# Kernel optimization log

Hardware: AMD Instinct MI355X
Metric: run time of the kernel (lower is better)

Reference implementation:

```python
import jax, jax.numpy as jnp
import numpy as np

B, S, D, H, IT, V = 2, 1024, 1024, 8, 28, 50257
DH = D // H
EPS = jnp.float32(1.1920929e-07)  # torch RMSNorm default eps = finfo(float32).eps


def _rmsnorm(x, w):
    # torch nn.RMSNorm: x * rsqrt(mean(x^2) + eps) * weight
    ms = jnp.mean(jnp.square(x), axis=-1, keepdims=True)
    return x * jax.lax.rsqrt(ms + EPS) * w


def setup_inputs() -> dict:
    key = jax.random.key(0)
    ks = jax.random.split(key, 8)
    s = 0.02
    tokens = jax.random.randint(ks[0], (B, S), 0, V)
    embed = jax.random.normal(ks[1], (V, D), dtype=jnp.float32) * s
    Wk = jax.random.normal(ks[2], (D, D), dtype=jnp.float32) * s
    Wv = jax.random.normal(ks[3], (D, D), dtype=jnp.float32) * s
    Ws = jax.random.normal(ks[4], (D, D), dtype=jnp.float32) * s
    Wo = jax.random.normal(ks[5], (D, D), dtype=jnp.float32) * s  # original zero-inits; randomized for a non-trivial baseline
    step_size = jnp.linspace(0.5, 0.1, IT, dtype=jnp.float32)
    norm_w = jnp.ones((IT, D), jnp.float32)   # per-iteration RMSNorm weight
    gamma = jnp.ones((IT, D), jnp.float32)
    beta = jnp.zeros((IT, D), jnp.float32)
    out_norm_w = jnp.ones((D,), jnp.float32)
    lm_head_w = jax.random.normal(ks[6], (V, D), dtype=jnp.float32) * s
    return dict(tokens=tokens, embed=embed, Wk=Wk, Wv=Wv, Ws=Ws, Wo=Wo,
                step_size=step_size, norm_w=norm_w, gamma=gamma, beta=beta,
                out_norm_w=out_norm_w, lm_head_w=lm_head_w)


def _forward(tokens, embed, Wk, Wv, Ws, Wo, step_size, norm_w, gamma, beta, out_norm_w, lm_head_w):
    b, s = tokens.shape
    causal = jnp.tril(jnp.ones((s, s), dtype=bool))  # allow j <= i
    scale = 1.0 / np.sqrt(DH)

    def compute_force(h):
        k = (h @ Wk.T).reshape(b, s, H, DH)
        v = (h @ Wv.T).reshape(b, s, H, DH)
        energy = jnp.einsum('bihd,bjhd->bhij', k, k) * scale
        logits = jnp.where(causal, -energy, -jnp.inf)  # softmax(-energy) with causal masking
        w = jax.nn.softmax(logits, axis=-1)
        pairwise = jnp.einsum('bhij,bjhd->bihd', w, v).reshape(b, s, D)
        return (pairwise + h @ Ws.T) @ Wo.T

    def step(x, p):
        st, nw, g, bb = p
        h = _rmsnorm(x, nw) * g + bb
        return x + compute_force(h) * st, None

    x0 = embed[tokens].astype(jnp.float32)
    x, _ = jax.lax.scan(jax.checkpoint(step), x0, (step_size, norm_w, gamma, beta))
    x = _rmsnorm(x, out_norm_w)
    return x @ lm_head_w.T  # [B, S, V] logits


def reference(tokens, embed, Wk, Wv, Ws, Wo, step_size, norm_w, gamma, beta, out_norm_w, lm_head_w):
    return _forward(tokens, embed, Wk, Wv, Ws, Wo, step_size, norm_w, gamma, beta, out_norm_w, lm_head_w)
```

## Files before the change

### kernel.cpp

```cpp
#include <hip/hip_runtime.h>
#include <cstdint>
#include <cstddef>

#define S_   1024
#define D_   1024
#define H_   8
#define DH_  128
#define IT_  28
#define V_   50257
#define B_   2
#define ROWS 2048
#define EPS_ 1.1920929e-07f

typedef unsigned short u16;
typedef __attribute__((ext_vector_type(8))) short s8v;
typedef __attribute__((ext_vector_type(4))) float f4v;

#define VMCNT0 asm volatile("s_waitcnt vmcnt(0)" ::: "memory")
#define LGKM0  asm volatile("s_waitcnt lgkmcnt(0)" ::: "memory")
#define RBAR   do { __builtin_amdgcn_s_barrier(); asm volatile("" ::: "memory"); } while (0)

static __device__ __forceinline__ void gload16(const void* g, void* l) {
  __builtin_amdgcn_global_load_lds((__attribute__((address_space(1))) void*)(g),
                                   (__attribute__((address_space(3))) void*)(l), 16, 0, 0);
}

static __device__ __forceinline__ u16 f2bf(float f) {
  union { float f; uint32_t u; } v; v.f = f;
  return (u16)((v.u + 0x7FFFu + ((v.u >> 16) & 1u)) >> 16);
}

static __device__ __forceinline__ float wave_sum(float v) {
#pragma unroll
  for (int o = 32; o > 0; o >>= 1) v += __shfl_xor(v, o, 64);
  return v;
}

__device__ __constant__ int IT_TAB[40] = {
  15,15,15,15, 14,14,14, 13,13,13, 12,12,12, 11,11,11,
  10,10, 9,9, 8,8, 7,7, 6, 5, 4, 3,
  14,10,6,2, 13,9,5,1, 12,8,4,0};
__device__ __constant__ int CH_TAB[40] = {
  0,1,2,3, 0,1,2, 0,1,2, 0,1,2, 0,1,2,
  0,1, 0,1, 0,1, 0,1, 0, 0, 0, 0,
  3,2,1,0, 3,2,1,0, 3,2,1,0};

__global__ __launch_bounds__(256) void k_embed(const int* __restrict__ tok,
                                               const float* __restrict__ emb,
                                               float* __restrict__ x) {
  const int row = blockIdx.x;
  const int t = tok[row];
  ((float4*)(x + (size_t)row * D_))[threadIdx.x] =
      ((const float4*)(emb + (size_t)t * D_))[threadIdx.x];
}

__global__ __launch_bounds__(256) void k_cvt(const float* __restrict__ w,
                                             u16* __restrict__ o, int n4) {
  const int idx = blockIdx.x * 256 + threadIdx.x;
  if (idx < n4) {
    const float4 f = ((const float4*)w)[idx];
    ushort4 u;
    u.x = f2bf(f.x); u.y = f2bf(f.y); u.z = f2bf(f.z); u.w = f2bf(f.w);
    ((ushort4*)o)[idx] = u;
  }
}

__global__ __launch_bounds__(256) void k_rmsnorm(const float* __restrict__ x,
                                                 const float* __restrict__ nw,
                                                 const float* __restrict__ g,
                                                 const float* __restrict__ bb,
                                                 u16* __restrict__ h) {
  const int row = blockIdx.x;
  const int tid = threadIdx.x;
  const float4 xv = ((const float4*)(x + (size_t)row * D_))[tid];
  float ss = xv.x*xv.x + xv.y*xv.y + xv.z*xv.z + xv.w*xv.w;
  ss = wave_sum(ss);
  __shared__ float red[4];
  const int lane = tid & 63, wid = tid >> 6;
  if (lane == 0) red[wid] = ss;
  __syncthreads();
  const float tot = red[0] + red[1] + red[2] + red[3];
  const float r = rsqrtf(tot * (1.0f / (float)D_) + EPS_);
  const float4 wv = ((const float4*)nw)[tid];
  float o[4];
  o[0] = xv.x * r * wv.x; o[1] = xv.y * r * wv.y;
  o[2] = xv.z * r * wv.z; o[3] = xv.w * r * wv.w;
  if (g) {
    const float4 gv = ((const float4*)g)[tid];
    const float4 bv = ((const float4*)bb)[tid];
    o[0] = o[0]*gv.x + bv.x; o[1] = o[1]*gv.y + bv.y;
    o[2] = o[2]*gv.z + bv.z; o[3] = o[3]*gv.w + bv.w;
  }
  ushort4 u;
  u.x = f2bf(o[0]); u.y = f2bf(o[1]); u.z = f2bf(o[2]); u.w = f2bf(o[3]);
  ((ushort4*)(h + (size_t)row * D_))[tid] = u;
}

template<int EPI, int SWAP, int NB>
__global__ __launch_bounds__(256) void k_gemm(const u16* __restrict__ A, int lda,
                                              const u16* __restrict__ Bm, int ldb,
                                              float* __restrict__ C, int ldc,
                                              int N, int K,
                                              const float* __restrict__ alphap, int aidx) {
  __shared__ u16 As0[128 * 32], As1[128 * 32];
  __shared__ u16 Bs0[64 * NB * 32], Bs1[64 * NB * 32];
  const int i0 = (SWAP ? blockIdx.x : blockIdx.y) * 128;
  const int j0 = (SWAP ? blockIdx.y : blockIdx.x) * (64 * NB);
  const int tid = threadIdx.x;
  const int lane = tid & 63, w = tid >> 6;
  const int wr = w >> 1, wc = w & 1;
  const int l15 = lane & 15, l4 = lane >> 4;
  const int ar = tid >> 2, ak = (tid & 3) << 3;
  int bj0 = j0 + ar;      if (bj0 > N - 1) bj0 = N - 1;
  int bj1 = j0 + ar + 64; if (bj1 > N - 1) bj1 = N - 1;

  f4v acc[4][2 * NB];
#pragma unroll
  for (int m = 0; m < 4; ++m)
#pragma unroll
    for (int n = 0; n < 2 * NB; ++n) acc[m][n] = (f4v)0.0f;

  auto STAGE = [&](u16* AsB, u16* BsB, int k0) {
    gload16(A + (size_t)(i0 + ar) * lda + k0 + ak, AsB + (size_t)tid * 8);
    gload16(A + (size_t)(i0 + ar + 64) * lda + k0 + ak, AsB + ((size_t)tid + 256) * 8);
    gload16(Bm + (size_t)bj0 * ldb + k0 + ak, BsB + (size_t)tid * 8);
    if (NB == 2)
      gload16(Bm + (size_t)bj1 * ldb + k0 + ak, BsB + ((size_t)tid + 256) * 8);
  };
  auto COMP = [&](const u16* AsB, const u16* BsB) {
    s8v a[4], b[2 * NB];
#pragma unroll
    for (int m = 0; m < 4; ++m)
      a[m] = *(const s8v*)&AsB[(wr * 64 + m * 16 + l15) * 32 + l4 * 8];
#pragma unroll
    for (int n = 0; n < 2 * NB; ++n)
      b[n] = *(const s8v*)&BsB[(wc * 32 * NB + n * 16 + l15) * 32 + l4 * 8];
    LGKM0;
#pragma unroll
    for (int m = 0; m < 4; ++m)
#pragma unroll
      for (int n = 0; n < 2 * NB; ++n)
        acc[m][n] = __builtin_amdgcn_mfma_f32_16x16x32_bf16(a[m], b[n], acc[m][n], 0, 0, 0);
  };

  STAGE(As0, Bs0, 0);
  VMCNT0;
  RBAR;

  for (int k0 = 0; k0 < K; k0 += 64) {
    STAGE(As1, Bs1, k0 + 32);
    COMP(As0, Bs0);
    VMCNT0;
    RBAR;
    if (k0 + 64 < K) STAGE(As0, Bs0, k0 + 64);
    COMP(As1, Bs1);
    VMCNT0;
    RBAR;
  }

  const float alpha = alphap ? alphap[aidx] : 1.0f;
#pragma unroll
  for (int m = 0; m < 4; ++m) {
#pragma unroll
    for (int n = 0; n < 2 * NB; ++n) {
      const int i = i0 + wr * 64 + m * 16 + l4 * 4;
      const int j = j0 + wc * 32 * NB + n * 16 + l15;
      const f4v v = acc[m][n];
      if (EPI == 0) {
        if (j < N) {
#pragma unroll
          for (int r = 0; r < 4; ++r) C[(size_t)(i + r) * ldc + j] = v[r];
        }
      } else {
#pragma unroll
        for (int r = 0; r < 4; ++r) C[(size_t)(i + r) * ldc + j] += alpha * v[r];
      }
    }
  }
}

__global__ __launch_bounds__(256) void k_gemm_qkv(const u16* __restrict__ A,
                                                  const u16* __restrict__ Wcat,
                                                  u16* __restrict__ kb,
                                                  u16* __restrict__ vt,
                                                  float* __restrict__ fb) {
  __shared__ u16 As0[128 * 32], As1[128 * 32];
  __shared__ u16 Bs0[64 * 32], Bs1[64 * 32];
  const int i0 = blockIdx.y * 128, j0 = blockIdx.x * 64;
  const int tid = threadIdx.x;
  const int lane = tid & 63, w = tid >> 6;
  const int wr = w >> 1, wc = w & 1;
  const int l15 = lane & 15, l4 = lane >> 4;
  const int ar = tid >> 2, ak = (tid & 3) << 3;

  f4v acc[4][2];
#pragma unroll
  for (int m = 0; m < 4; ++m)
#pragma unroll
    for (int n = 0; n < 2; ++n) acc[m][n] = (f4v)0.0f;

  auto STAGE = [&](u16* AsB, u16* BsB, int k0) {
    gload16(A + (size_t)(i0 + ar) * D_ + k0 + ak, AsB + (size_t)tid * 8);
    gload16(A + (size_t)(i0 + ar + 64) * D_ + k0 + ak, AsB + ((size_t)tid + 256) * 8);
    gload16(Wcat + (size_t)(j0 + ar) * D_ + k0 + ak, BsB + (size_t)tid * 8);
  };
  auto COMP = [&](const u16* AsB, const u16* BsB) {
    s8v a[4], b[2];
#pragma unroll
    for (int m = 0; m < 4; ++m)
      a[m] = *(const s8v*)&AsB[(wr * 64 + m * 16 + l15) * 32 + l4 * 8];
#pragma unroll
    for (int n = 0; n < 2; ++n)
      b[n] = *(const s8v*)&BsB[(wc * 32 + n * 16 + l15) * 32 + l4 * 8];
    LGKM0;
#pragma unroll
    for (int m = 0; m < 4; ++m)
#pragma unroll
      for (int n = 0; n < 2; ++n)
        acc[m][n] = __builtin_amdgcn_mfma_f32_16x16x32_bf16(a[m], b[n], acc[m][n], 0, 0, 0);
  };

  STAGE(As0, Bs0, 0);
  VMCNT0;
  RBAR;
  for (int k0 = 0; k0 < D_; k0 += 64) {
    STAGE(As1, Bs1, k0 + 32);
    COMP(As0, Bs0);
    VMCNT0;
    RBAR;
    if (k0 + 64 < D_) STAGE(As0, Bs0, k0 + 64);
    COMP(As1, Bs1);
    VMCNT0;
    RBAR;
  }

#pragma unroll
  for (int m = 0; m < 4; ++m) {
#pragma unroll
    for (int n = 0; n < 2; ++n) {
      const int i = i0 + wr * 64 + m * 16 + l4 * 4;
      const int j = j0 + wc * 32 + n * 16 + l15;
      const int sel = j >> 10, jl = j & 1023;
      const f4v v = acc[m][n];
      if (sel == 0) {
#pragma unroll
        for (int r = 0; r < 4; ++r) kb[(size_t)(i + r) * D_ + jl] = f2bf(v[r]);
      } else if (sel == 1) {
        ushort4 p;
        p.x = f2bf(v[0]); p.y = f2bf(v[1]); p.z = f2bf(v[2]); p.w = f2bf(v[3]);
        *(ushort4*)&vt[((size_t)(i >> 10) * D_ + jl) * S_ + (i & 1023)] = p;
      } else {
#pragma unroll
        for (int r = 0; r < 4; ++r) fb[(size_t)(i + r) * D_ + jl] = v[r];
      }
    }
  }
}

__global__ __launch_bounds__(256) void k_attn_part(const u16* __restrict__ kb,
                                                   const u16* __restrict__ vt,
                                                   float* __restrict__ po,
                                                   float* __restrict__ pml,
                                                   float scale) {
  const int it = IT_TAB[blockIdx.x], ch = CH_TAB[blockIdx.x];
  const int z = blockIdx.y;
  const int b = z >> 3, h = z & 7;
  const u16* Kbh = kb + (size_t)b * S_ * D_ + h * DH_;
  const u16* Vth = vt + ((size_t)b * D_ + h * DH_) * S_;
  const int i0 = it * 64;
  const int jt0 = ch * 4;
  const int jtend = min(jt0 + 4, it + 1);
  __shared__ u16 Kj[64 * 128];
  __shared__ u16 Vj[128 * 64];
  __shared__ u16 Pl[4][16 * 64];
  const int tid = threadIdx.x;
  const int lane = tid & 63, w = tid >> 6;
  const int l15 = lane & 15, l4 = lane >> 4;

  s8v ka[4];
#pragma unroll
  for (int ks = 0; ks < 4; ++ks)
    ka[ks] = *(const s8v*)(Kbh + (size_t)(i0 + w * 16 + l15) * D_ + ks * 32 + l4 * 8);

  f4v acc_o[8];
#pragma unroll
  for (int n = 0; n < 8; ++n) acc_o[n] = (f4v)0.0f;
  float mrow[4], lrow[4];
#pragma unroll
  for (int r = 0; r < 4; ++r) { mrow[r] = -3.0e38f; lrow[r] = 0.f; }

  const int krow = tid >> 4, koff = (tid & 15) * 8;
  const int vrow = tid >> 3, voff = (tid & 7) * 8;

  for (int jt = jt0; jt < jtend; ++jt) {
    const int j0 = jt * 64;
#pragma unroll
    for (int p = 0; p < 4; ++p) {
      const int row = p * 16 + krow;
      gload16(Kbh + (size_t)(j0 + row) * D_ + (koff ^ ((row & 7) << 3)),
              &Kj[(size_t)(p * 256 + tid) * 8]);
    }
#pragma unroll
    for (int p = 0; p < 4; ++p) {
      const int row = p * 32 + vrow;
      gload16(Vth + (size_t)row * S_ + j0 + (voff ^ ((row & 7) << 3)),
              &Vj[(size_t)(p * 256 + tid) * 8]);
    }
    __syncthreads();

    f4v s[4];
#pragma unroll
    for (int n = 0; n < 4; ++n) s[n] = (f4v)0.0f;
#pragma unroll
    for (int ks = 0; ks < 4; ++ks) {
#pragma unroll
      for (int n = 0; n < 4; ++n) {
        const int row = n * 16 + l15;
        const s8v kf = *(const s8v*)&Kj[row * 128 + ((ks * 32 + l4 * 8) ^ ((row & 7) << 3))];
        s[n] = __builtin_amdgcn_mfma_f32_16x16x32_bf16(ka[ks], kf, s[n], 0, 0, 0);
      }
    }

    float pv[4][4], tmax[4];
#pragma unroll
    for (int r = 0; r < 4; ++r) tmax[r] = -3.0e38f;
#pragma unroll
    for (int n = 0; n < 4; ++n) {
      const int j = j0 + n * 16 + l15;
#pragma unroll
      for (int r = 0; r < 4; ++r) {
        const int i = i0 + w * 16 + l4 * 4 + r;
        const float lg = (j <= i) ? (-scale * s[n][r]) : -3.0e38f;
        pv[n][r] = lg;
        tmax[r] = fmaxf(tmax[r], lg);
      }
    }
#pragma unroll
    for (int r = 0; r < 4; ++r) {
#pragma unroll
      for (int o = 8; o > 0; o >>= 1) tmax[r] = fmaxf(tmax[r], __shfl_xor(tmax[r], o, 64));
    }
    float es[4];
#pragma unroll
    for (int r = 0; r < 4; ++r) {
      const float mn = fmaxf(mrow[r], tmax[r]);
      es[r] = __expf(mrow[r] - mn);
      mrow[r] = mn;
    }
    float psum[4] = {0.f, 0.f, 0.f, 0.f};
#pragma unroll
    for (int n = 0; n < 4; ++n) {
#pragma unroll
      for (int r = 0; r < 4; ++r) {
        const float p = __expf(pv[n][r] - mrow[r]);
        pv[n][r] = p;
        psum[r] += p;
      }
    }
#pragma unroll
    for (int r = 0; r < 4; ++r) {
#pragma unroll
      for (int o = 8; o > 0; o >>= 1) psum[r] += __shfl_xor(psum[r], o, 64);
      lrow[r] = lrow[r] * es[r] + psum[r];
    }
#pragma unroll
    for (int n = 0; n < 8; ++n) {
      f4v t = acc_o[n];
      t[0] *= es[0]; t[1] *= es[1]; t[2] *= es[2]; t[3] *= es[3];
      acc_o[n] = t;
    }

    u16* P = Pl[w];
#pragma unroll
    for (int n = 0; n < 4; ++n) {
#pragma unroll
      for (int r = 0; r < 4; ++r) {
        const int row = l4 * 4 + r;
        P[row * 64 + ((n * 16 + l15) ^ ((row & 7) << 3))] = f2bf(pv[n][r]);
      }
    }
    __syncthreads();
    s8v pa[2];
#pragma unroll
    for (int kp = 0; kp < 2; ++kp)
      pa[kp] = *(const s8v*)&P[l15 * 64 + ((kp * 32 + l4 * 8) ^ ((l15 & 7) << 3))];

#pragma unroll
    for (int kp = 0; kp < 2; ++kp) {
#pragma unroll
      for (int n = 0; n < 8; ++n) {
        const int d = n * 16 + l15;
        const s8v vf = *(const s8v*)&Vj[d * 64 + ((kp * 32 + l4 * 8) ^ ((d & 7) << 3))];
        acc_o[n] = __builtin_amdgcn_mfma_f32_16x16x32_bf16(pa[kp], vf, acc_o[n], 0, 0, 0);
      }
    }
    __syncthreads();
  }

  const int slot = (z * 16 + it) * 4 + ch;
  float* O = po + (size_t)slot * (64 * 128);
#pragma unroll
  for (int n = 0; n < 8; ++n) {
#pragma unroll
    for (int r = 0; r < 4; ++r)
      O[(w * 16 + l4 * 4 + r) * 128 + n * 16 + l15] = acc_o[n][r];
  }
  if (l15 == 0) {
#pragma unroll
    for (int r = 0; r < 4; ++r) {
      const int row = w * 16 + l4 * 4 + r;
      pml[(size_t)slot * 128 + row] = mrow[r];
      pml[(size_t)slot * 128 + 64 + row] = lrow[r];
    }
  }
}

__global__ __launch_bounds__(256) void k_attn_merge(const float* __restrict__ po,
                                                    const float* __restrict__ pml,
                                                    const float* __restrict__ fb,
                                                    u16* __restrict__ fbh) {
  const int it = blockIdx.x, z = blockIdx.y;
  const int b = z >> 3, h = z & 7;
  const int nch = (it >> 2) + 1;
  const int row = threadIdx.x >> 2;
  const int cseg = (threadIdx.x & 3) * 32;
  const int base = (z * 16 + it) * 4;

  float ms = -3.0e38f, mv[4], lv[4];
#pragma unroll
  for (int c = 0; c < 4; ++c)
    if (c < nch) {
      mv[c] = pml[(size_t)(base + c) * 128 + row];
      lv[c] = pml[(size_t)(base + c) * 128 + 64 + row];
      ms = fmaxf(ms, mv[c]);
    }
  float ls = 0.f, fac[4];
#pragma unroll
  for (int c = 0; c < 4; ++c)
    if (c < nch) { fac[c] = __expf(mv[c] - ms); ls += lv[c] * fac[c]; }
  const float inv = 1.0f / ls;

  float4 o[8];
#pragma unroll
  for (int q = 0; q < 8; ++q) o[q] = make_float4(0.f, 0.f, 0.f, 0.f);
#pragma unroll
  for (int c = 0; c < 4; ++c)
    if (c < nch) {
      const float4* Oc = (const float4*)(po + (size_t)(base + c) * (64 * 128) + row * 128 + cseg);
      const float f = fac[c];
#pragma unroll
      for (int q = 0; q < 8; ++q) {
        const float4 t = Oc[q];
        o[q].x += t.x * f; o[q].y += t.y * f; o[q].z += t.z * f; o[q].w += t.w * f;
      }
    }

  const size_t gidx = ((size_t)(b * S_ + it * 64 + row)) * D_ + h * DH_ + cseg;
  const float4* F = (const float4*)(fb + gidx);
  u16* out = fbh + gidx;
#pragma unroll
  for (int q = 0; q < 8; ++q) {
    const float4 fv = F[q];
    ushort4 u;
    u.x = f2bf(fv.x + o[q].x * inv);
    u.y = f2bf(fv.y + o[q].y * inv);
    u.z = f2bf(fv.z + o[q].z * inv);
    u.w = f2bf(fv.w + o[q].w * inv);
    *(ushort4*)(out + q * 4) = u;
  }
}

extern "C" void kernel_launch(void* const* d_in, const int* in_sizes, int n_in,
                              void* d_out, int out_size, void* d_ws, size_t ws_size,
                              hipStream_t stream) {
  const int*   tok = (const int*)  d_in[0];
  const float* emb = (const float*)d_in[1];
  const float* Wk  = (const float*)d_in[2];
  const float* Wv  = (const float*)d_in[3];
  const float* Ws  = (const float*)d_in[4];
  const float* Wo  = (const float*)d_in[5];
  const float* stp = (const float*)d_in[6];
  const float* nw  = (const float*)d_in[7];
  const float* gam = (const float*)d_in[8];
  const float* bet = (const float*)d_in[9];
  const float* onw = (const float*)d_in[10];
  const float* lmw = (const float*)d_in[11];
  float* out = (float*)d_out;

  uint8_t* wsb = (uint8_t*)d_ws;
  float* x   = (float*)wsb;  wsb += (size_t)ROWS * D_ * 4;
  u16* hb    = (u16*)wsb;    wsb += (size_t)ROWS * D_ * 2;
  u16* kb    = (u16*)wsb;    wsb += (size_t)ROWS * D_ * 2;
  u16* vt    = (u16*)wsb;    wsb += (size_t)ROWS * D_ * 2;
  float* fb  = (float*)wsb;  wsb += (size_t)ROWS * D_ * 4;
  u16* fbh   = (u16*)wsb;    wsb += (size_t)ROWS * D_ * 2;
  u16* Wcat  = (u16*)wsb;    wsb += (size_t)3 * D_ * D_ * 2;
  u16* Wob   = (u16*)wsb;    wsb += (size_t)D_ * D_ * 2;
  float* po  = (float*)wsb;  wsb += (size_t)1024 * 64 * 128 * 4;
  float* pml = (float*)wsb;  wsb += (size_t)1024 * 128 * 4;
  u16* Wlm   = (u16*)wsb;    wsb += (size_t)V_ * D_ * 2;

  const float scale = 0.08838834764831845f;
  const int n4 = D_ * D_ / 4;

  k_cvt<<<1024, 256, 0, stream>>>(Wk, Wcat, n4);
  k_cvt<<<1024, 256, 0, stream>>>(Wv, Wcat + (size_t)D_ * D_, n4);
  k_cvt<<<1024, 256, 0, stream>>>(Ws, Wcat + (size_t)2 * D_ * D_, n4);
  k_cvt<<<1024, 256, 0, stream>>>(Wo, Wob, n4);
  k_embed<<<ROWS, 256, 0, stream>>>(tok, emb, x);

  for (int it = 0; it < IT_; ++it) {
    k_rmsnorm<<<ROWS, 256, 0, stream>>>(x, nw + (size_t)it * D_,
                                        gam + (size_t)it * D_, bet + (size_t)it * D_, hb);
    k_gemm_qkv<<<dim3(48, 16), 256, 0, stream>>>(hb, Wcat, kb, vt, fb);
    k_attn_part<<<dim3(40, 16), 256, 0, stream>>>(kb, vt, po, pml, scale);
    k_attn_merge<<<dim3(16, 16), 256, 0, stream>>>(po, pml, fb, fbh);
    k_gemm<1, 0, 1><<<dim3(16, 16), 256, 0, stream>>>(fbh, D_, Wob, D_, x, D_, D_, D_, stp, it);
  }

  k_rmsnorm<<<ROWS, 256, 0, stream>>>(x, onw, nullptr, nullptr, hb);

  k_cvt<<<(V_ * 256 + 255) / 256, 256, 0, stream>>>(lmw, Wlm, V_ * D_ / 4);
  k_gemm<0, 1, 2><<<dim3(16, (V_ + 127) / 128), 256, 0, stream>>>(hb, D_, Wlm, D_, out, V_, V_, D_,
                                                                  nullptr, 0);
}
```

Measured before the change: 2.861 ms.

## Triple-buffer GEMM LDS staging with partial vmcnt waits

Both GEMM kernels move from double-buffered LDS staging, which waited on all outstanding loads every step, to a three-stage ring. Up to two future K-slices stay in flight, and each step waits with a partial s_waitcnt vmcnt matched to the per-stage load count. This lets global loads overlap several MFMA compute steps, hiding more memory latency. In exchange it uses 50% more shared memory, which may reduce occupancy, and the hardcoded vmcnt values must match the number of loads issued per STAGE.

```diff
diff --git a/kernel.cpp b/kernel.cpp
--- a/kernel.cpp
+++ b/kernel.cpp
@@ -102,8 +102,8 @@
                                               float* __restrict__ C, int ldc,
                                               int N, int K,
                                               const float* __restrict__ alphap, int aidx) {
-  __shared__ u16 As0[128 * 32], As1[128 * 32];
-  __shared__ u16 Bs0[64 * NB * 32], Bs1[64 * NB * 32];
+  __shared__ u16 As0[128 * 32], As1[128 * 32], As2[128 * 32];
+  __shared__ u16 Bs0[64 * NB * 32], Bs1[64 * NB * 32], Bs2[64 * NB * 32];
   const int i0 = (SWAP ? blockIdx.x : blockIdx.y) * 128;
   const int j0 = (SWAP ? blockIdx.y : blockIdx.x) * (64 * NB);
   const int tid = threadIdx.x;
@@ -142,20 +142,34 @@
       for (int n = 0; n < 2 * NB; ++n)
         acc[m][n] = __builtin_amdgcn_mfma_f32_16x16x32_bf16(a[m], b[n], acc[m][n], 0, 0, 0);
   };
-
+  auto WAIT = [&](int ahead) {
+    if (NB == 2) {
+      if (ahead >= 2)      asm volatile("s_waitcnt vmcnt(8)" ::: "memory");
+      else if (ahead == 1) asm volatile("s_waitcnt vmcnt(4)" ::: "memory");
+      else                 VMCNT0;
+    } else {
+      if (ahead >= 2)      asm volatile("s_waitcnt vmcnt(6)" ::: "memory");
+      else if (ahead == 1) asm volatile("s_waitcnt vmcnt(3)" ::: "memory");
+      else                 VMCNT0;
+    }
+  };
+
+  const int nk = K >> 5;
   STAGE(As0, Bs0, 0);
-  VMCNT0;
-  RBAR;
-
-  for (int k0 = 0; k0 < K; k0 += 64) {
-    STAGE(As1, Bs1, k0 + 32);
-    COMP(As0, Bs0);
-    VMCNT0;
+  STAGE(As1, Bs1, 32);
+  STAGE(As2, Bs2, 64);
+  for (int i = 0; i < nk; ++i) {
+    u16 *Asb, *Bsb;
+    const int m3 = i % 3;
+    if (m3 == 0) { Asb = As0; Bsb = Bs0; }
+    else if (m3 == 1) { Asb = As1; Bsb = Bs1; }
+    else { Asb = As2; Bsb = Bs2; }
+    const int rem = nk - 1 - i;
+    WAIT(rem < 2 ? rem : 2);
     RBAR;
-    if (k0 + 64 < K) STAGE(As0, Bs0, k0 + 64);
-    COMP(As1, Bs1);
-    VMCNT0;
+    COMP(Asb, Bsb);
     RBAR;
+    if (i + 3 < nk) STAGE(Asb, Bsb, (i + 3) << 5);
   }
 
   const float alpha = alphap ? alphap[aidx] : 1.0f;
@@ -184,8 +198,8 @@
                                                   u16* __restrict__ kb,
                                                   u16* __restrict__ vt,
                                                   float* __restrict__ fb) {
-  __shared__ u16 As0[128 * 32], As1[128 * 32];
-  __shared__ u16 Bs0[64 * 32], Bs1[64 * 32];
+  __shared__ u16 As0[128 * 32], As1[128 * 32], As2[128 * 32];
+  __shared__ u16 Bs0[64 * 32], Bs1[64 * 32], Bs2[64 * 32];
   const int i0 = blockIdx.y * 128, j0 = blockIdx.x * 64;
   const int tid = threadIdx.x;
   const int lane = tid & 63, w = tid >> 6;
@@ -219,19 +233,28 @@
       for (int n = 0; n < 2; ++n)
         acc[m][n] = __builtin_amdgcn_mfma_f32_16x16x32_bf16(a[m], b[n], acc[m][n], 0, 0, 0);
   };
-
+  auto WAIT = [&](int ahead) {
+    if (ahead >= 2)      asm volatile("s_waitcnt vmcnt(6)" ::: "memory");
+    else if (ahead == 1) asm volatile("s_waitcnt vmcnt(3)" ::: "memory");
+    else                 VMCNT0;
+  };
+
+  const int nk = D_ >> 5;
   STAGE(As0, Bs0, 0);
-  VMCNT0;
-  RBAR;
-  for (int k0 = 0; k0 < D_; k0 += 64) {
-    STAGE(As1, Bs1, k0 + 32);
-    COMP(As0, Bs0);
-    VMCNT0;
+  STAGE(As1, Bs1, 32);
+  STAGE(As2, Bs2, 64);
+  for (int i = 0; i < nk; ++i) {
+    u16 *Asb, *Bsb;
+    const int m3 = i % 3;
+    if (m3 == 0) { Asb = As0; Bsb = Bs0; }
+    else if (m3 == 1) { Asb = As1; Bsb = Bs1; }
+    else { Asb = As2; Bsb = Bs2; }
+    const int rem = nk - 1 - i;
+    WAIT(rem < 2 ? rem : 2);
     RBAR;
-    if (k0 + 64 < D_) STAGE(As0, Bs0, k0 + 64);
-    COMP(As1, Bs1);
-    VMCNT0;
+    COMP(Asb, Bsb);
     RBAR;
+    if (i + 3 < nk) STAGE(Asb, Bsb, (i + 3) << 5);
   }
 
 #pragma unroll
```

Measured after the change: 2.849 ms. No clear change (-0.4%).
